# Optimization experiments

Hardware: AMD Instinct MI355X
Metric: run time of the kernel (lower is better)

The kernel has to match this reference:

```python
import jax, jax.numpy as jnp
import numpy as np

K = 32          # neighbors
DIV = 4         # division
S = K // DIV    # maxpool window
EPS = 1e-5      # BatchNorm eps (torch default)


def _bn_last(x, g, b):
    # BatchNorm over channel = last axis, training-mode batch stats (biased var),
    # equivalent to torch's transpose->BatchNorm2d->transpose in Dense(in_dim=4).
    m = x.mean(axis=(0, 1, 2), keepdims=True)
    v = x.var(axis=(0, 1, 2), keepdims=True)
    return (x - m) / jnp.sqrt(v + EPS) * g + b


def setup_inputs() -> dict:
    key = jax.random.key(0)
    ks = jax.random.split(key, 16)
    B, N, M, F1, F2 = 8, 4096, 2048, 128, 256
    Fmid = 64
    Cin = Fmid + F1  # 192
    inp = {
        "points": jax.random.normal(ks[0], (B, N, 3), dtype=jnp.float32),
        "queries": jax.random.normal(ks[1], (B, M, 3), dtype=jnp.float32),
        "prev_features": jax.random.normal(ks[2], (B, N, F1), dtype=jnp.float32),
        # dense1: 3 -> 32
        "g1": jnp.ones((3,), jnp.float32),
        "b1": jnp.zeros((3,), jnp.float32),
        "W1": jax.random.normal(ks[3], (3, Fmid // 2), dtype=jnp.float32) * 0.3,
        "c1": jnp.zeros((Fmid // 2,), jnp.float32),
        # dense2: 32 -> 64
        "g2": jnp.ones((Fmid // 2,), jnp.float32),
        "b2": jnp.zeros((Fmid // 2,), jnp.float32),
        "W2": jax.random.normal(ks[4], (Fmid // 2, Fmid), dtype=jnp.float32) * 0.1,
        "c2": jnp.zeros((Fmid,), jnp.float32),
        # conv block: BN2d(192) + Conv2d(192 -> 256, kernel (1,4))
        "g3": jnp.ones((Cin,), jnp.float32),
        "b3": jnp.zeros((Cin,), jnp.float32),
        "Wc": jax.random.normal(ks[5], (F2, Cin, DIV), dtype=jnp.float32) * 0.05,
        "bc": jnp.zeros((F2,), jnp.float32),
    }
    return inp


def reference(points, queries, prev_features, g1, b1, W1, c1, g2, b2, W2, c2,
              g3, b3, Wc, bc):
    B, N, _ = points.shape
    M = queries.shape[1]

    # --- KNN: negative squared distance, topk largest = k nearest ---
    # dist[b,m,n] = -||q-p||^2 = 2 q.p - ||q||^2 - ||p||^2
    dist = (2.0 * jnp.einsum('bmd,bnd->bmn', queries, points)
            - jnp.sum(queries ** 2, -1)[:, :, None]
            - jnp.sum(points ** 2, -1)[:, None, :])
    _, idx = jax.lax.top_k(dist, K)  # (B, M, K) int32

    gather = jax.vmap(lambda feats, i: feats[i])  # (N,F),(M,K) -> (M,K,F)
    knn_pts = gather(points, idx)                 # (B, M, K, 3)

    # local coords: center - neighbor
    local = queries[:, :, None, :] - knn_pts       # (B, M, K, 3)

    # dense1 / dense2: BN -> Linear -> ReLU
    h = jax.nn.relu(_bn_last(local, g1, b1) @ W1 + c1)  # (B,M,K,32)
    h = jax.nn.relu(_bn_last(h, g2, b2) @ W2 + c2)      # (B,M,K,64)

    # gather previous features, concat
    prev_k = gather(prev_features, idx)                 # (B,M,K,F1)
    feat = jnp.concatenate([h, prev_k], axis=-1)        # (B,M,K,192)

    # permute to NCHW, maxpool (1,S) stride S over K -> width DIV
    x = jnp.transpose(feat, (0, 3, 1, 2))               # (B,C,M,K)
    C = x.shape[1]
    x = x.reshape(B, C, M, DIV, S).max(axis=-1)         # (B,C,M,DIV)

    # BN2d over channel (training-mode batch stats)
    m = x.mean(axis=(0, 2, 3), keepdims=True)
    v = x.var(axis=(0, 2, 3), keepdims=True)
    x = (x - m) / jnp.sqrt(v + EPS) * g3[None, :, None, None] + b3[None, :, None, None]

    # Conv2d kernel (1,DIV) collapses width to 1: contraction over (C, DIV)
    out = jnp.einsum('bcmd,ocd->bmo', x, Wc) + bc       # (B,M,F2)
    return jax.nn.relu(out)
```

## Files before the change

### kernel.cpp

```cpp
#include <hip/hip_runtime.h>
#include <hip/hip_bf16.h>
#include <math.h>


#define B_   8
#define N_   4096
#define M_   2048
#define K_   32
#define F1_  128
#define F2_  256
#define CIN_ 192
#define NROWS_ (B_*M_*K_)
#define NQ_    (B_*M_)
#define EPS_ 1e-5f

#define S2_BLK 64
#define S3_BLK 512

typedef __attribute__((ext_vector_type(8))) short bf16x8;
typedef __attribute__((ext_vector_type(4))) float f32x4;

__device__ __forceinline__ unsigned int fkey(float qx, float qy, float qz, float qq,
                                             float x, float y, float z) {
    float dot = fmaf(qz, z, fmaf(qy, y, __fmul_rn(qx, x)));
    float pp  = __fadd_rn(__fadd_rn(__fmul_rn(x, x), __fmul_rn(y, y)), __fmul_rn(z, z));
    float d   = __fsub_rn(__fsub_rn(__fmul_rn(2.0f, dot), qq), pp);
    unsigned int u = __float_as_uint(d);
    return u ^ ((unsigned int)((int)u >> 31) | 0x80000000u);
}

__device__ __forceinline__ unsigned int pack_hi(float f0, float f1) {
    return (__float_as_uint(f0) >> 16) | (__float_as_uint(f1) & 0xFFFF0000u);
}
__device__ __forceinline__ unsigned int pack_lo(float f0, float f1) {
    float r0 = f0 - __uint_as_float(__float_as_uint(f0) & 0xFFFF0000u);
    float r1 = f1 - __uint_as_float(__float_as_uint(f1) & 0xFFFF0000u);
    return (__float_as_uint(r0) >> 16) | (__float_as_uint(r1) & 0xFFFF0000u);
}

__global__ __launch_bounds__(512) void knn_kernel(const float* __restrict__ points,
                                                  const float* __restrict__ queries,
                                                  int* __restrict__ idx_out,
                                                  float* __restrict__ local_out,
                                                  float* __restrict__ part1) {
    __shared__ float px[4160], py[4160], pz[4160];
    __shared__ float acc1[8][6];
    const int q0 = blockIdx.x * 8;
    const int b  = q0 >> 11;
    const float* pb = points + (size_t)b * N_ * 3;
    for (int p = threadIdx.x; p < N_; p += 512) {
        const float* g = pb + p * 3;
        int a = (p >> 6) * 65 + (p & 63);
        px[a] = g[0]; py[a] = g[1]; pz[a] = g[2];
    }
    __syncthreads();

    const int lane = threadIdx.x & 63;
    const int wid  = threadIdx.x >> 6;
    const int q = q0 + wid;
    const float qx = queries[q * 3 + 0];
    const float qy = queries[q * 3 + 1];
    const float qz = queries[q * 3 + 2];
    const float qq = __fadd_rn(__fadd_rn(__fmul_rn(qx, qx), __fmul_rn(qy, qy)), __fmul_rn(qz, qz));

    unsigned int m_fk = 0u, bj = 0u;
    #pragma unroll 8
    for (unsigned int j = 0; j < 64; ++j) {
        int a = (int)j * 65 + lane;
        unsigned int fk = fkey(qx, qy, qz, qq, px[a], py[a], pz[a]);
        if (fk > m_fk) { m_fk = fk; bj = j; }
    }
    unsigned int m_n = (unsigned int)lane + (bj << 6);

    unsigned long long takenT = 0ull;
    int sel_n = 0;
    const int rb = lane * 65;
    for (int r = 0; r < 32; ++r) {
        unsigned int g = m_fk;
        #pragma unroll
        for (int off = 32; off; off >>= 1) {
            unsigned int o = __shfl_xor(g, off, 64);
            g = (o > g) ? o : g;
        }
        unsigned long long mk = __ballot(m_fk == g);
        unsigned int nstar;
        if (__popcll(mk) == 1) {
            int src = __ffsll(mk) - 1;
            nstar = (unsigned int)__shfl((int)m_n, src, 64);
        } else {
            unsigned int nm = (m_fk == g) ? m_n : 0xFFFFFFFFu;
            #pragma unroll
            for (int off = 32; off; off >>= 1) {
                unsigned int o = __shfl_xor(nm, off, 64);
                nm = (o < nm) ? o : nm;
            }
            nstar = nm;
        }
        if (lane == r) sel_n = (int)nstar;
        const int w  = nstar & 63;
        const int js = (int)(nstar >> 6);
        if (lane == js) takenT |= (1ull << w);
        int a2 = rb + w;
        unsigned int fk2 = fkey(qx, qy, qz, qq, px[a2], py[a2], pz[a2]);
        if ((unsigned int)(takenT >> w) & 1u) fk2 = 0u;
        unsigned int g2 = fk2;
        #pragma unroll
        for (int off = 32; off; off >>= 1) {
            unsigned int o = __shfl_xor(g2, off, 64);
            g2 = (o > g2) ? o : g2;
        }
        unsigned long long mk2 = __ballot(fk2 == g2);
        int src2 = __ffsll(mk2) - 1;
        if (lane == w) { m_fk = g2; m_n = (unsigned int)(w + (src2 << 6)); }
    }

    float vx = 0.f, vy = 0.f, vz = 0.f;
    if (lane < 32) {
        idx_out[q * K_ + lane] = sel_n;
        int a = (sel_n >> 6) * 65 + (sel_n & 63);
        vx = __fsub_rn(qx, px[a]);
        vy = __fsub_rn(qy, py[a]);
        vz = __fsub_rn(qz, pz[a]);
        size_t o = ((size_t)q * K_ + lane) * 3;
        local_out[o + 0] = vx; local_out[o + 1] = vy; local_out[o + 2] = vz;
    }
    float s0 = vx, s1 = vy, s2 = vz, s3 = vx*vx, s4 = vy*vy, s5 = vz*vz;
    #pragma unroll
    for (int off = 32; off; off >>= 1) {
        s0 += __shfl_xor(s0, off, 64); s1 += __shfl_xor(s1, off, 64);
        s2 += __shfl_xor(s2, off, 64); s3 += __shfl_xor(s3, off, 64);
        s4 += __shfl_xor(s4, off, 64); s5 += __shfl_xor(s5, off, 64);
    }
    if (lane == 0) { acc1[wid][0]=s0; acc1[wid][1]=s1; acc1[wid][2]=s2;
                     acc1[wid][3]=s3; acc1[wid][4]=s4; acc1[wid][5]=s5; }
    __syncthreads();
    if (threadIdx.x < 6) {
        float s = 0.f;
        #pragma unroll
        for (int i = 0; i < 8; ++i) s += acc1[i][threadIdx.x];
        part1[blockIdx.x * 8 + threadIdx.x] = s;
    }
}

__global__ __launch_bounds__(256) void fold1_kernel(const float* __restrict__ part1,
                             const float* __restrict__ g1, const float* __restrict__ b1,
                             const float* __restrict__ W1, const float* __restrict__ c1,
                             float* __restrict__ W1p, float* __restrict__ c1p) {
    __shared__ float red[32][8];
    __shared__ float cs[8];
    const int t = threadIdx.x;
    const int c = t & 7, ch = t >> 3;
    float s = 0.f;
    for (int i = 0; i < 64; ++i) s += part1[(ch * 64 + i) * 8 + c];
    red[ch][c] = s;
    __syncthreads();
    if (t < 8) {
        float v = 0.f;
        #pragma unroll
        for (int i = 0; i < 32; ++i) v += red[i][t];
        cs[t] = v;
    }
    __syncthreads();
    if (t >= 32) return;
    const float inv_n = 1.0f / (float)NROWS_;
    float cacc = c1[t];
    #pragma unroll
    for (int c3 = 0; c3 < 3; ++c3) {
        float mean = cs[c3] * inv_n;
        float var  = cs[3 + c3] * inv_n - mean * mean;
        float sc   = g1[c3] / sqrtf(var + EPS_);
        float tc   = b1[c3] - mean * sc;
        float w    = W1[c3 * 32 + t];
        W1p[c3 * 32 + t] = sc * w;
        cacc += tc * w;
    }
    c1p[t] = cacc;
}

__global__ __launch_bounds__(256) void stats2_kernel(const float* __restrict__ local,
                                                     const float* __restrict__ W1p,
                                                     const float* __restrict__ c1p,
                                                     float* __restrict__ part2) {
    __shared__ float w[96], cb[32];
    __shared__ float red[4][64];
    if (threadIdx.x < 96) w[threadIdx.x] = W1p[threadIdx.x];
    if (threadIdx.x < 32) cb[threadIdx.x] = c1p[threadIdx.x];
    __syncthreads();
    float sum[32], sq[32];
    #pragma unroll
    for (int i = 0; i < 32; ++i) { sum[i] = 0.f; sq[i] = 0.f; }
    int tid = blockIdx.x * 256 + threadIdx.x;
    for (int r = tid; r < NROWS_; r += S2_BLK * 256) {
        float x = local[(size_t)r*3], y = local[(size_t)r*3+1], z = local[(size_t)r*3+2];
        #pragma unroll
        for (int f = 0; f < 32; ++f) {
            float h = fmaf(z, w[64 + f], fmaf(y, w[32 + f], fmaf(x, w[f], cb[f])));
            h = fmaxf(h, 0.0f);
            sum[f] += h; sq[f] += h * h;
        }
    }
    #pragma unroll
    for (int f = 0; f < 32; ++f) {
        #pragma unroll
        for (int off = 32; off; off >>= 1) {
            sum[f] += __shfl_xor(sum[f], off, 64);
            sq[f]  += __shfl_xor(sq[f], off, 64);
        }
    }
    int lane = threadIdx.x & 63, wid = threadIdx.x >> 6;
    if (lane == 0) {
        #pragma unroll
        for (int f = 0; f < 32; ++f) { red[wid][f] = sum[f]; red[wid][32 + f] = sq[f]; }
    }
    __syncthreads();
    if (threadIdx.x < 64) {
        part2[blockIdx.x * 64 + threadIdx.x] =
            red[0][threadIdx.x] + red[1][threadIdx.x] + red[2][threadIdx.x] + red[3][threadIdx.x];
    }
}

__global__ void fold2_kernel(const float* __restrict__ part2,
                             const float* __restrict__ g2, const float* __restrict__ b2,
                             const float* __restrict__ W2, const float* __restrict__ c2,
                             float* __restrict__ W2p, float* __restrict__ c2p) {
    __shared__ float cs[64];
    int f = threadIdx.x;
    {
        float s = 0.f;
        for (int i = 0; i < S2_BLK; ++i) s += part2[i * 64 + f];
        cs[f] = s;
    }
    __syncthreads();
    const float inv_n = 1.0f / (float)NROWS_;
    float cacc = c2[f];
    for (int c = 0; c < 32; ++c) {
        float mean = cs[c] * inv_n;
        float var  = cs[32 + c] * inv_n - mean * mean;
        float sc   = g2[c] / sqrtf(var + EPS_);
        float tc   = b2[c] - mean * sc;
        float wv   = W2[c * 64 + f];
        W2p[c * 64 + f] = sc * wv;
        cacc += tc * wv;
    }
    c2p[f] = cacc;
}

__global__ __launch_bounds__(256) void h2pool_kernel(const float* __restrict__ local,
                                                     const float* __restrict__ W1p,
                                                     const float* __restrict__ c1p,
                                                     const float* __restrict__ W2p,
                                                     const float* __restrict__ c2p,
                                                     float* __restrict__ xp) {
    __shared__ float h1buf[4][32 * 32];
    const int lane = threadIdx.x & 63, wid = threadIdx.x >> 6;
    const int q = blockIdx.x * 4 + wid;

    float w2c[32];
    #pragma unroll 8
    for (int c = 0; c < 32; ++c) w2c[c] = W2p[c * 64 + lane];
    const float c2l = c2p[lane];

    const int f0 = lane & 31;
    const float wa = W1p[f0], wb = W1p[32 + f0], wc = W1p[64 + f0], cc = c1p[f0];
    float* hb = &h1buf[wid][0];
    #pragma unroll 2
    for (int i = 0; i < 16; ++i) {
        int t = lane + 64 * i;
        int k = t >> 5;
        size_t lo = ((size_t)q * K_ + k) * 3;
        float x = local[lo], y = local[lo + 1], z = local[lo + 2];
        float h = fmaf(z, wc, fmaf(y, wb, fmaf(x, wa, cc)));
        hb[t] = fmaxf(h, 0.0f);
    }
    __syncthreads();

    float pm[4] = {-INFINITY, -INFINITY, -INFINITY, -INFINITY};
    #pragma unroll 2
    for (int k = 0; k < 32; ++k) {
        const float* hk = &hb[k * 32];
        float acc = c2l;
        #pragma unroll
        for (int c = 0; c < 32; ++c) acc = fmaf(hk[c], w2c[c], acc);
        float h2 = fmaxf(acc, 0.0f);
        int g = k >> 3;
        pm[g] = fmaxf(pm[g], h2);
    }

    float* xq = xp + (size_t)q * 4 * CIN_;
    #pragma unroll
    for (int g = 0; g < 4; ++g) xq[g * CIN_ + lane] = pm[g];
}

__global__ __launch_bounds__(256) void gatherpool_kernel(const int* __restrict__ idx,
                                                         const float* __restrict__ prev,
                                                         float* __restrict__ xp) {
    const int lane = threadIdx.x & 63, wid = threadIdx.x >> 6;
    const int bid = blockIdx.x;
    const int q = ((bid & 7) << 11) + ((bid >> 3) << 2) + wid;
    const int b = q >> 11;

    int iv = 0;
    if (lane < 32) iv = idx[q * K_ + lane];
    float p0[4] = {-INFINITY, -INFINITY, -INFINITY, -INFINITY};
    float p1[4] = {-INFINITY, -INFINITY, -INFINITY, -INFINITY};
    const float* pbase = prev + (size_t)b * N_ * F1_;
    #pragma unroll 4
    for (int k = 0; k < 32; ++k) {
        int row = __shfl(iv, k, 64);
        const float* pr = pbase + (size_t)row * F1_;
        float v0 = pr[lane];
        float v1 = pr[64 + lane];
        int g = k >> 3;
        p0[g] = fmaxf(p0[g], v0);
        p1[g] = fmaxf(p1[g], v1);
    }

    float* xq = xp + (size_t)q * 4 * CIN_;
    #pragma unroll
    for (int g = 0; g < 4; ++g) {
        xq[g * CIN_ + 64 + lane]  = p0[g];
        xq[g * CIN_ + 128 + lane] = p1[g];
    }
}

__global__ __launch_bounds__(192) void stats3_kernel(const float* __restrict__ xp,
                                                     float* __restrict__ part3) {
    int c = threadIdx.x;
    int r0 = blockIdx.x * 128;
    float s = 0.f, sq = 0.f;
    #pragma unroll 4
    for (int i = 0; i < 128; ++i) {
        float v = xp[(size_t)(r0 + i) * CIN_ + c];
        s += v; sq += v * v;
    }
    part3[blockIdx.x * 384 + c]       = s;
    part3[blockIdx.x * 384 + 192 + c] = sq;
}

__global__ __launch_bounds__(384) void finalize3_kernel(const float* __restrict__ part3,
                                                        float* __restrict__ stats3) {
    int t = threadIdx.x;
    float s = 0.f;
    for (int i = 0; i < S3_BLK; ++i) s += part3[i * 384 + t];
    stats3[t] = s;
}

__global__ __launch_bounds__(256) void fold3_kernel(const float* __restrict__ stats3,
                                                    const float* __restrict__ g3, const float* __restrict__ b3,
                                                    const float* __restrict__ Wc, const float* __restrict__ bc,
                                                    unsigned short* __restrict__ Wh,
                                                    unsigned short* __restrict__ Wl,
                                                    float* __restrict__ bcp) {
    const int o = blockIdx.x;
    const float inv_n = 1.0f / (float)(NQ_ * 4);
    __shared__ float red[256];
    float tacc = 0.f;
    for (int t = threadIdx.x; t < CIN_ * 4; t += 256) {
        int c = t >> 2, d = t & 3;
        float mean = stats3[c] * inv_n;
        float var  = stats3[192 + c] * inv_n - mean * mean;
        float sc   = g3[c] / sqrtf(var + EPS_);
        float tc   = b3[c] - mean * sc;
        float wv   = Wc[(size_t)o * (CIN_ * 4) + t];
        float w    = sc * wv;
        unsigned int u = __float_as_uint(w);
        float rr = w - __uint_as_float(u & 0xFFFF0000u);
        int f  = d * CIN_ + c;
        int ks = f >> 5, j = f & 7, lg = (f >> 3) & 3;
        size_t fi = ((size_t)(ks * 16 + (o >> 4)) * 64 + (lg * 16 + (o & 15))) * 8 + j;
        Wh[fi] = (unsigned short)(u >> 16);
        Wl[fi] = (unsigned short)(__float_as_uint(rr) >> 16);
        tacc += tc * wv;
    }
    red[threadIdx.x] = tacc;
    __syncthreads();
    for (int s = 128; s; s >>= 1) {
        if (threadIdx.x < s) red[threadIdx.x] += red[threadIdx.x + s];
        __syncthreads();
    }
    if (threadIdx.x == 0) bcp[o] = bc[o] + red[0];
}

__global__ __launch_bounds__(512) void conv_kernel(const float* __restrict__ xp,
                                                   const unsigned short* __restrict__ Wh,
                                                   const unsigned short* __restrict__ Wl,
                                                   const float* __restrict__ bcp,
                                                   float* __restrict__ out) {
    __shared__ __align__(16) unsigned short Ah_s[64 * 64];
    __shared__ __align__(16) unsigned short Al_s[64 * 64];
    __shared__ __align__(16) unsigned short Bh_s[2 * 16 * 64 * 8];
    __shared__ __align__(16) unsigned short Bl_s[2 * 16 * 64 * 8];

    const int tid  = threadIdx.x;
    const int lane = tid & 63;
    const int wid  = tid >> 6;
    const int wr   = wid >> 2;
    const int wc   = wid & 3;
    const int row0 = blockIdx.x * 64;

    f32x4 acc[2][4];
    #pragma unroll
    for (int i = 0; i < 2; ++i)
        #pragma unroll
        for (int n = 0; n < 4; ++n) acc[i][n] = (f32x4){0.f, 0.f, 0.f, 0.f};

    const int ar  = tid >> 3;
    const int akq = tid & 7;
    const int a_byte = ar * 128 + ((akq ^ (ar & 7)) << 4);
    const float* arow = xp + (size_t)(row0 + ar) * 768 + akq * 8;

    const int fr_row = lane & 15;
    const int fr_grp = lane >> 4;

    for (int ks2 = 0; ks2 < 12; ++ks2) {
        __syncthreads();
        {
            const float* p = arow + ks2 * 64;
            float4 v0 = *(const float4*)p;
            float4 v1 = *(const float4*)(p + 4);
            uint4 h4, l4;
            h4.x = pack_hi(v0.x, v0.y); h4.y = pack_hi(v0.z, v0.w);
            h4.z = pack_hi(v1.x, v1.y); h4.w = pack_hi(v1.z, v1.w);
            l4.x = pack_lo(v0.x, v0.y); l4.y = pack_lo(v0.z, v0.w);
            l4.z = pack_lo(v1.x, v1.y); l4.w = pack_lo(v1.z, v1.w);
            *(uint4*)((char*)Ah_s + a_byte) = h4;
            *(uint4*)((char*)Al_s + a_byte) = l4;
        }
        {
            const uint4* gh = (const uint4*)(Wh + (size_t)ks2 * 16384);
            const uint4* gl = (const uint4*)(Wl + (size_t)ks2 * 16384);
            uint4* lh = (uint4*)Bh_s;
            uint4* ll = (uint4*)Bl_s;
            #pragma unroll
            for (int i = 0; i < 4; ++i) {
                lh[tid + 512 * i] = gh[tid + 512 * i];
                ll[tid + 512 * i] = gl[tid + 512 * i];
            }
        }
        __syncthreads();
        #pragma unroll
        for (int ks = 0; ks < 2; ++ks) {
            bf16x8 ah[2], al[2];
            #pragma unroll
            for (int i = 0; i < 2; ++i) {
                int r = wr * 32 + i * 16 + fr_row;
                int slot = ks * 4 + fr_grp;
                int byte = r * 128 + ((slot ^ (r & 7)) << 4);
                ah[i] = *(const bf16x8*)((const char*)Ah_s + byte);
                al[i] = *(const bf16x8*)((const char*)Al_s + byte);
            }
            #pragma unroll
            for (int nt = 0; nt < 4; ++nt) {
                int bidx = ((ks * 16 + wc * 4 + nt) * 64 + lane) * 8;
                bf16x8 bh = *(const bf16x8*)(Bh_s + bidx);
                bf16x8 bl = *(const bf16x8*)(Bl_s + bidx);
                #pragma unroll
                for (int i = 0; i < 2; ++i) {
                    acc[i][nt] = __builtin_amdgcn_mfma_f32_16x16x32_bf16(ah[i], bh, acc[i][nt], 0, 0, 0);
                    acc[i][nt] = __builtin_amdgcn_mfma_f32_16x16x32_bf16(ah[i], bl, acc[i][nt], 0, 0, 0);
                    acc[i][nt] = __builtin_amdgcn_mfma_f32_16x16x32_bf16(al[i], bh, acc[i][nt], 0, 0, 0);
                }
            }
        }
    }

    float bias[4];
    #pragma unroll
    for (int nt = 0; nt < 4; ++nt) bias[nt] = bcp[wc * 64 + nt * 16 + fr_row];
    #pragma unroll
    for (int i = 0; i < 2; ++i) {
        #pragma unroll
        for (int nt = 0; nt < 4; ++nt) {
            int col = wc * 64 + nt * 16 + fr_row;
            #pragma unroll
            for (int rg = 0; rg < 4; ++rg) {
                int row = row0 + wr * 32 + i * 16 + fr_grp * 4 + rg;
                out[(size_t)row * F2_ + col] = fmaxf(acc[i][nt][rg] + bias[nt], 0.0f);
            }
        }
    }
}

extern "C" void kernel_launch(void* const* d_in, const int* in_sizes, int n_in,
                              void* d_out, int out_size, void* d_ws, size_t ws_size,
                              hipStream_t stream) {
    const float* points  = (const float*)d_in[0];
    const float* queries = (const float*)d_in[1];
    const float* prev    = (const float*)d_in[2];
    const float* g1 = (const float*)d_in[3];
    const float* b1 = (const float*)d_in[4];
    const float* W1 = (const float*)d_in[5];
    const float* c1 = (const float*)d_in[6];
    const float* g2 = (const float*)d_in[7];
    const float* b2 = (const float*)d_in[8];
    const float* W2 = (const float*)d_in[9];
    const float* c2 = (const float*)d_in[10];
    const float* g3 = (const float*)d_in[11];
    const float* b3 = (const float*)d_in[12];
    const float* Wc = (const float*)d_in[13];
    const float* bc = (const float*)d_in[14];
    float* out = (float*)d_out;

    char* ws = (char*)d_ws;
    size_t off_idx    = 0;
    size_t off_local  = off_idx + (size_t)NQ_*K_*4;
    size_t off_stats3 = off_local + (size_t)NROWS_*3*4;
    size_t off_W1p    = off_stats3 + 4096;
    size_t off_c1p    = off_W1p + 512;
    size_t off_W2p    = off_c1p + 512;
    size_t off_c2p    = off_W2p + 8192;
    size_t off_Wt     = off_c2p + 512;
    size_t off_bcp    = off_Wt + 786432;
    size_t off_xp     = off_bcp + 1024;

    int*   idx    = (int*)(ws + off_idx);
    float* local  = (float*)(ws + off_local);
    float* stats3 = (float*)(ws + off_stats3);
    float* W1p    = (float*)(ws + off_W1p);
    float* c1p    = (float*)(ws + off_c1p);
    float* W2p    = (float*)(ws + off_W2p);
    float* c2p    = (float*)(ws + off_c2p);
    unsigned short* Wh = (unsigned short*)(ws + off_Wt);
    unsigned short* Wl = (unsigned short*)(ws + off_Wt + 393216);
    float* bcp    = (float*)(ws + off_bcp);
    float* xp     = (float*)(ws + off_xp);
    float* part1  = (float*)(ws + off_Wt);
    float* part2  = (float*)(ws + off_Wt + 65536);
    float* part3  = (float*)(ws + off_local);

    knn_kernel<<<NQ_ / 8, 512, 0, stream>>>(points, queries, idx, local, part1);
    fold1_kernel<<<1, 256, 0, stream>>>(part1, g1, b1, W1, c1, W1p, c1p);
    stats2_kernel<<<S2_BLK, 256, 0, stream>>>(local, W1p, c1p, part2);
    fold2_kernel<<<1, 64, 0, stream>>>(part2, g2, b2, W2, c2, W2p, c2p);
    h2pool_kernel<<<NQ_ / 4, 256, 0, stream>>>(local, W1p, c1p, W2p, c2p, xp);
    gatherpool_kernel<<<NQ_ / 4, 256, 0, stream>>>(idx, prev, xp);
    stats3_kernel<<<S3_BLK, 192, 0, stream>>>(xp, part3);
    finalize3_kernel<<<1, 384, 0, stream>>>(part3, stats3);
    fold3_kernel<<<F2_, 256, 0, stream>>>(stats3, g3, b3, Wc, bc, Wh, Wl, bcp);
    conv_kernel<<<NQ_ / 64, 512, 0, stream>>>(xp, Wh, Wl, bcp, out);
}
```

Before: 416.2 us.

## Keep top-two candidates per lane in KNN selection and retune stats partitioning

Each lane in the KNN kernel now tracks its two best candidates as packed 64-bit keys (distance plus inverted index), so a selected lane usually promotes its second-best instead of rescanning its column and doing an extra wave reduction. The rescan only runs when a lane's backup is exhausted. Separately, the partial-sum block counts for the stats2 and stats3 reductions are rebalanced and their final reduction loops unrolled. This costs a few more registers and compares in the initial scan, and tie-breaking now depends on the packed index encoding.

```diff
diff --git a/kernel.cpp b/kernel.cpp
--- a/kernel.cpp
+++ b/kernel.cpp
@@ -14,8 +14,9 @@
 #define NQ_    (B_*M_)
 #define EPS_ 1e-5f
 
-#define S2_BLK 64
-#define S3_BLK 512
+#define S2_BLK 512
+#define S3_BLK 128
+#define S3_ROWS (65536 / S3_BLK)
 
 typedef __attribute__((ext_vector_type(8))) short bf16x8;
 typedef __attribute__((ext_vector_type(4))) float f32x4;
@@ -63,19 +64,25 @@
     const float qz = queries[q * 3 + 2];
     const float qq = __fadd_rn(__fadd_rn(__fmul_rn(qx, qx), __fmul_rn(qy, qy)), __fmul_rn(qz, qz));
 
-    unsigned int m_fk = 0u, bj = 0u;
-    #pragma unroll 8
+    unsigned long long m0 = 0ull, m1 = 0ull;
+    #pragma unroll 4
     for (unsigned int j = 0; j < 64; ++j) {
         int a = (int)j * 65 + lane;
         unsigned int fk = fkey(qx, qy, qz, qq, px[a], py[a], pz[a]);
-        if (fk > m_fk) { m_fk = fk; bj = j; }
-    }
-    unsigned int m_n = (unsigned int)lane + (bj << 6);
+        unsigned long long key = ((unsigned long long)fk << 32)
+                               | (unsigned int)~((unsigned int)lane + (j << 6));
+        if (key > m1) {
+            unsigned long long lo = (key < m0) ? key : m0;
+            m0 = (key > m0) ? key : m0;
+            m1 = lo;
+        }
+    }
 
     unsigned long long takenT = 0ull;
     int sel_n = 0;
     const int rb = lane * 65;
     for (int r = 0; r < 32; ++r) {
+        unsigned int m_fk = (unsigned int)(m0 >> 32);
         unsigned int g = m_fk;
         #pragma unroll
         for (int off = 32; off; off >>= 1) {
@@ -86,9 +93,9 @@
         unsigned int nstar;
         if (__popcll(mk) == 1) {
             int src = __ffsll(mk) - 1;
-            nstar = (unsigned int)__shfl((int)m_n, src, 64);
+            nstar = ~(unsigned int)__shfl((int)(unsigned int)m0, src, 64);
         } else {
-            unsigned int nm = (m_fk == g) ? m_n : 0xFFFFFFFFu;
+            unsigned int nm = (m_fk == g) ? ~(unsigned int)m0 : 0xFFFFFFFFu;
             #pragma unroll
             for (int off = 32; off; off >>= 1) {
                 unsigned int o = __shfl_xor(nm, off, 64);
@@ -100,18 +107,25 @@
         const int w  = nstar & 63;
         const int js = (int)(nstar >> 6);
         if (lane == js) takenT |= (1ull << w);
-        int a2 = rb + w;
-        unsigned int fk2 = fkey(qx, qy, qz, qq, px[a2], py[a2], pz[a2]);
-        if ((unsigned int)(takenT >> w) & 1u) fk2 = 0u;
-        unsigned int g2 = fk2;
-        #pragma unroll
-        for (int off = 32; off; off >>= 1) {
-            unsigned int o = __shfl_xor(g2, off, 64);
-            g2 = (o > g2) ? o : g2;
-        }
-        unsigned long long mk2 = __ballot(fk2 == g2);
-        int src2 = __ffsll(mk2) - 1;
-        if (lane == w) { m_fk = g2; m_n = (unsigned int)(w + (src2 << 6)); }
+        if (lane == w) { m0 = m1; m1 = 0ull; }
+        unsigned long long need = __ballot(lane == w && m0 == 0ull);
+        if (need) {
+            int a2 = rb + w;
+            unsigned int fk2 = fkey(qx, qy, qz, qq, px[a2], py[a2], pz[a2]);
+            if ((unsigned int)(takenT >> w) & 1u) fk2 = 0u;
+            unsigned int g2 = fk2;
+            #pragma unroll
+            for (int off = 32; off; off >>= 1) {
+                unsigned int o = __shfl_xor(g2, off, 64);
+                g2 = (o > g2) ? o : g2;
+            }
+            unsigned long long mk2 = __ballot(fk2 == g2);
+            int src2 = __ffsll(mk2) - 1;
+            if (lane == w) {
+                m0 = ((unsigned long long)g2 << 32)
+                   | (unsigned int)~((unsigned int)w + ((unsigned int)src2 << 6));
+            }
+        }
     }
 
     float vx = 0.f, vy = 0.f, vz = 0.f;
@@ -227,6 +241,7 @@
     int f = threadIdx.x;
     {
         float s = 0.f;
+        #pragma unroll 8
         for (int i = 0; i < S2_BLK; ++i) s += part2[i * 64 + f];
         cs[f] = s;
     }
@@ -326,10 +341,10 @@
 __global__ __launch_bounds__(192) void stats3_kernel(const float* __restrict__ xp,
                                                      float* __restrict__ part3) {
     int c = threadIdx.x;
-    int r0 = blockIdx.x * 128;
+    int r0 = blockIdx.x * S3_ROWS;
     float s = 0.f, sq = 0.f;
     #pragma unroll 4
-    for (int i = 0; i < 128; ++i) {
+    for (int i = 0; i < S3_ROWS; ++i) {
         float v = xp[(size_t)(r0 + i) * CIN_ + c];
         s += v; sq += v * v;
     }
@@ -341,6 +356,7 @@
                                                         float* __restrict__ stats3) {
     int t = threadIdx.x;
     float s = 0.f;
+    #pragma unroll 4
     for (int i = 0; i < S3_BLK; ++i) s += part3[i * 384 + t];
     stats3[t] = s;
 }
```

New measurement: 420.6 us. Within noise of the previous version (+1.1%).
